# Kernel tuning notes

Hardware: AMD Instinct MI355X
Metric: run time of the kernel (lower is better)

The kernel has to match this reference:

```python
import jax, jax.numpy as jnp
import numpy as np

N_EVENTS = 16384
B = 4
H = W = 64
KH = KW = 3
P = KH * KW
D = 256  # input_size == hidden_size


def setup_inputs() -> dict:
    rng = np.random.default_rng(0)
    # events sorted by batch, time = arange (sorted within batch)
    batch_id = np.sort(rng.integers(0, B, N_EVENTS))
    hh = rng.integers(KH - 1, H - KH + 1, N_EVENTS)  # interior pixels -> exactly P patches each
    ww = rng.integers(KW - 1, W - KW + 1, N_EVENTS)
    time = np.arange(N_EVENTS)
    # scatter each event to its P=kh*kw overlapping patches (stride 1)
    Hp, Wp = H - KH + 1, W - KW + 1
    ki = np.arange(KH)[:, None]
    kj = np.arange(KW)[None, :]
    pos = (ki * KW + kj).reshape(1, P)                       # [1, P]
    pl = hh[:, None] - ki.reshape(1, -1).repeat(KW, 1).reshape(1, P) if False else None
    ki_f = np.repeat(np.arange(KH), KW)                       # [P]
    kj_f = np.tile(np.arange(KW), KH)                         # [P]
    patch_row = hh[:, None] - ki_f[None, :]                   # [N, P]
    patch_col = ww[:, None] - kj_f[None, :]
    patch_lin = (batch_id[:, None] * (Hp * Wp) + patch_row * Wp + patch_col).reshape(-1)
    pos_flat = np.broadcast_to((ki_f * KW + kj_f)[None, :], (N_EVENTS, P)).reshape(-1)
    orig_flat = np.repeat(np.arange(N_EVENTS), P)
    t_flat = np.repeat(time, P)
    order = np.lexsort((t_flat, patch_lin))                   # group by patch, time-ordered within
    patch_sorted = patch_lin[order]
    orig_event_idx = orig_flat[order].astype(np.int32)
    pos_id = pos_flat[order].astype(np.int32)
    seg_start = np.concatenate([[True], patch_sorted[1:] != patch_sorted[:-1]])

    key = jax.random.key(0)
    ks = jax.random.split(key, 8)
    std = np.sqrt(2.0 / (D + D)).astype(np.float32)
    lin = 1.0 / np.sqrt(D).astype(np.float32)
    return {
        "events": jax.random.normal(ks[0], (N_EVENTS, D), jnp.float32),
        "scatter_w": jax.random.normal(ks[1], (P, D, D), jnp.float32) * std,
        "gather_w": jax.random.normal(ks[2], (P, D, D), jnp.float32) * std,
        "q_w": jax.random.normal(ks[3], (D, D), jnp.float32) * lin,
        "v_w": jax.random.normal(ks[4], (D, D), jnp.float32) * lin,
        "g_w": jax.random.normal(ks[5], (D, D), jnp.float32) * lin,
        "o_w": jax.random.normal(ks[6], (D, D), jnp.float32) * lin,
        "ln_gamma": jnp.ones((D,), jnp.float32),
        "ln_beta": jnp.zeros((D,), jnp.float32),
        "orig_event_idx": jnp.asarray(orig_event_idx),
        "pos_id": jnp.asarray(pos_id),
        "seg_start": jnp.asarray(seg_start),
    }


def _pos_proj(x, weights, pos_id):
    # per-patch-position linear: out[n] = weights[pos_id[n]] @ x[n]
    # disjoint masks partition rows, so masked GEMMs sum exactly (mirrors torch loop)
    out = jnp.zeros((x.shape[0], weights.shape[1]), x.dtype)
    for i in range(weights.shape[0]):
        m = (pos_id == i)[:, None]
        out = out + jnp.where(m, x @ weights[i].T, 0.0)
    return out


def _gated_scan(g, v, seg_start):
    # h_t = g_t * h_{t-1} + (1 - g_t) * v_t, reset at segment starts
    a = jnp.where(seg_start[:, None], 0.0, g)
    b = (1.0 - g) * v
    def comb(c1, c2):
        a1, b1 = c1
        a2, b2 = c2
        return (a1 * a2, a2 * b1 + b2)
    _, h = jax.lax.associative_scan(comb, (a, b), axis=0)
    return h


def reference(events, scatter_w, gather_w, q_w, v_w, g_w, o_w, ln_gamma, ln_beta,
              orig_event_idx, pos_id, seg_start):
    x = events[orig_event_idx]                     # [M, D] scatter events -> patch copies
    y = _pos_proj(x, scatter_w, pos_id)            # indexed conv-like projection
    q = y @ q_w.T
    v = y @ v_w.T
    g = jax.nn.sigmoid(y @ g_w.T)
    h = _gated_scan(g, v, seg_start)               # ragged gated linear scan
    o = (q * h) @ o_w.T
    z = _pos_proj(o, gather_w, pos_id)             # indexed gather projection
    out = jnp.zeros_like(events).at[orig_event_idx].add(z)  # gather back (sum over P copies)
    out = out + events                             # residual (input_size == hidden_size)
    mu = jnp.mean(out, axis=-1, keepdims=True)
    var = jnp.mean(jnp.square(out - mu), axis=-1, keepdims=True)
    out = (out - mu) * jax.lax.rsqrt(var + 1e-5) * ln_gamma + ln_beta
    return out
```

## Files before the change

### kernel.cpp

```cpp
#include <hip/hip_runtime.h>

typedef __bf16 bf16x8 __attribute__((ext_vector_type(8)));
typedef float f32x4 __attribute__((ext_vector_type(4)));

#define NEV 16384
#define MTOT 147456
#define LDQ 2304
#define LDX 6912

__device__ __forceinline__ unsigned short f2bf(float f) {
  unsigned x = __float_as_uint(f);
  x += 0x7FFFu + ((x >> 16) & 1u);
  return (unsigned short)(x >> 16);
}
__device__ __forceinline__ float bf2f(unsigned short u) {
  return __uint_as_float(((unsigned)u) << 16);
}
__device__ __forceinline__ void load_lds16(const void* g, void* l) {
  __builtin_amdgcn_global_load_lds(
      (const __attribute__((address_space(1))) unsigned int*)g,
      (__attribute__((address_space(3))) unsigned int*)l, 16, 0, 0);
}

__global__ void k_cast4(const float* __restrict__ in, unsigned short* __restrict__ out, int n4) {
  int i = blockIdx.x * blockDim.x + threadIdx.x;
  if (i >= n4) return;
  float4 v = reinterpret_cast<const float4*>(in)[i];
  ushort4 o;
  o.x = f2bf(v.x); o.y = f2bf(v.y); o.z = f2bf(v.z); o.w = f2bf(v.w);
  reinterpret_cast<ushort4*>(out)[i] = o;
}

__global__ void k_cast3(const float* __restrict__ q, const float* __restrict__ v,
                        const float* __restrict__ g, unsigned short* __restrict__ out) {
  int which = blockIdx.y;
  const float* src = (which == 0) ? q : (which == 1) ? v : g;
  int i = blockIdx.x * blockDim.x + threadIdx.x;
  if (i >= 16384) return;
  float4 val = reinterpret_cast<const float4*>(src)[i];
  ushort4 o;
  o.x = f2bf(val.x); o.y = f2bf(val.y); o.z = f2bf(val.z); o.w = f2bf(val.w);
  reinterpret_cast<ushort4*>(out + (long)which * 65536)[i] = o;
}

__global__ void k_transpose(const float* __restrict__ in, unsigned short* __restrict__ out, int total) {
  int i = blockIdx.x * blockDim.x + threadIdx.x;
  if (i >= total) return;
  int b = i >> 16, r = (i >> 8) & 255, c = i & 255;
  out[i] = f2bf(in[((long)b << 16) + (c << 8) + r]);
}

__global__ void k_detect(const unsigned int* __restrict__ seg, int* mode) {
  __shared__ int fFloat, fGt1;
  if (threadIdx.x == 0) { fFloat = 0; fGt1 = 0; }
  __syncthreads();
  int lf = 0, lg = 0;
  for (int i = threadIdx.x; i < 1024; i += 256) {
    unsigned v = seg[i];
    if (v == 0x3F800000u) lf = 1;
    else if (v > 1u) lg = 1;
  }
  if (lf) atomicOr(&fFloat, 1);
  if (lg) atomicOr(&fGt1, 1);
  __syncthreads();
  if (threadIdx.x == 0) *mode = fFloat ? 2 : (fGt1 ? 1 : 0);
}

__device__ __forceinline__ bool is_start(const void* seg, int mode, int i) {
  if (mode == 1) return ((const unsigned char*)seg)[i] != 0;
  if (mode == 2) return ((const float*)seg)[i] != 0.0f;
  return ((const int*)seg)[i] != 0;
}

__global__ void k_compact(const void* __restrict__ seg, const int* __restrict__ mode,
                          int* counter, int* starts) {
  int i = blockIdx.x * blockDim.x + threadIdx.x;
  if (i >= MTOT) return;
  if (is_start(seg, *mode, i)) {
    int k = atomicAdd(counter, 1);
    starts[k] = i;
  }
}

template<bool F32OUT>
__device__ __forceinline__ void gemm_tile(
    const unsigned short* __restrict__ A, const unsigned short* __restrict__ B,
    void* __restrict__ Cv, const float* __restrict__ resid,
    int r0, int c0, int K, int lda, int ldb, int ldc,
    unsigned short* As, unsigned short* Bs) {
  const int tid = threadIdx.x, lane = tid & 63, wid = tid >> 6;
  const int wr = (wid >> 1) * 64, wc = (wid & 1) * 64;
  const int la = lane & 15, lb2 = lane >> 4;
  const int arow = tid >> 2;
  const int cs = ((tid & 3) ^ ((arow >> 1) & 3)) * 8;
  const int nk = K >> 5;
  f32x4 acc[4][4];
#pragma unroll
  for (int i = 0; i < 4; ++i)
#pragma unroll
    for (int j = 0; j < 4; ++j) acc[i][j] = (f32x4)0.0f;

  const unsigned short* ga0 = A + (long)(r0 + arow) * lda + cs;
  const unsigned short* gb0 = B + (long)(c0 + arow) * ldb + cs;

  load_lds16(ga0, &As[tid * 8]);
  load_lds16(ga0 + (long)64 * lda, &As[2048 + tid * 8]);
  load_lds16(gb0, &Bs[tid * 8]);
  load_lds16(gb0 + (long)64 * ldb, &Bs[2048 + tid * 8]);
  __syncthreads();

  for (int k = 0; k < nk; ++k) {
    if (k + 1 < nk) {
      const int nb = ((k + 1) & 1) * 4096;
      const unsigned short* ga = ga0 + (k + 1) * 32;
      const unsigned short* gb = gb0 + (k + 1) * 32;
      load_lds16(ga, &As[nb + tid * 8]);
      load_lds16(ga + (long)64 * lda, &As[nb + 2048 + tid * 8]);
      load_lds16(gb, &Bs[nb + tid * 8]);
      load_lds16(gb + (long)64 * ldb, &Bs[nb + 2048 + tid * 8]);
    }
    const int cb = (k & 1) * 4096;
    bf16x8 af[4], bv[4];
#pragma unroll
    for (int i = 0; i < 4; ++i) {
      const int ra = wr + i * 16 + la;
      const int rb = wc + i * 16 + la;
      af[i] = *reinterpret_cast<const bf16x8*>(&As[cb + ra * 32 + ((lb2 ^ ((ra >> 1) & 3)) * 8)]);
      bv[i] = *reinterpret_cast<const bf16x8*>(&Bs[cb + rb * 32 + ((lb2 ^ ((rb >> 1) & 3)) * 8)]);
    }
#pragma unroll
    for (int i = 0; i < 4; ++i)
#pragma unroll
      for (int j = 0; j < 4; ++j)
        acc[i][j] = __builtin_amdgcn_mfma_f32_16x16x32_bf16(af[i], bv[j], acc[i][j], 0, 0, 0);
    __syncthreads();
  }
#pragma unroll
  for (int i = 0; i < 4; ++i)
#pragma unroll
    for (int j = 0; j < 4; ++j)
#pragma unroll
      for (int r = 0; r < 4; ++r) {
        const int row = r0 + wr + i * 16 + lb2 * 4 + r;
        const int col = c0 + wc + j * 16 + la;
        if (F32OUT) {
          float v = acc[i][j][r];
          if (resid) v += resid[(long)row * ldc + col];
          ((float*)Cv)[(long)row * ldc + col] = v;
        } else {
          ((unsigned short*)Cv)[(long)row * ldc + col] = f2bf(acc[i][j][r]);
        }
      }
}

__global__ __launch_bounds__(256) void k_wgemm(
    const unsigned short* __restrict__ qvgw, const unsigned short* __restrict__ wt,
    const unsigned short* __restrict__ gaw, const unsigned short* __restrict__ owt,
    unsigned short* __restrict__ ABig, unsigned short* __restrict__ Bo2) {
  __shared__ __align__(16) unsigned short As[8192];
  __shared__ __align__(16) unsigned short Bs[8192];
  const int b = blockIdx.z;
  const unsigned short *A, *B;
  unsigned short* C;
  int ldc;
  if (b < 27) {
    A = qvgw + (long)(b / 9) * 65536;
    B = wt + (long)(b % 9) * 65536;
    C = ABig + (long)b * 65536; ldc = 256;
  } else {
    A = gaw + (long)(b - 27) * 65536;
    B = owt;
    C = Bo2 + (b - 27) * 256; ldc = LDQ;
  }
  gemm_tile<false>(A, B, C, nullptr, blockIdx.x * 128, blockIdx.y * 128, 256, 256, 256, ldc, As, Bs);
}

__global__ __launch_bounds__(256) void k_qvg3(
    const unsigned short* __restrict__ ev, const unsigned short* __restrict__ ABig,
    unsigned short* __restrict__ X) {
  __shared__ __align__(16) unsigned short As[4096];
  __shared__ __align__(16) unsigned short Bs[3][2048];
  const int p = blockIdx.z;
  const int r0 = blockIdx.x * 128, c0 = blockIdx.y * 64;
  const int tid = threadIdx.x, lane = tid & 63, wid = tid >> 6;
  const int wr2 = (wid >> 1) * 64, wc2 = (wid & 1) * 32;
  const int la = lane & 15, lb2 = lane >> 4;
  f32x4 acc[3][4][2];
#pragma unroll
  for (int w = 0; w < 3; ++w)
#pragma unroll
    for (int i = 0; i < 4; ++i)
#pragma unroll
      for (int j = 0; j < 2; ++j) acc[w][i][j] = (f32x4)0.0f;

  for (int k0 = 0; k0 < 256; k0 += 32) {
#pragma unroll
    for (int q = 0; q < 2; ++q) {
      const int g = q * 256 + tid;
      const int row = g >> 2, c = g & 3;
      load_lds16(ev + (long)(r0 + row) * 256 + k0 + ((c ^ ((row >> 1) & 3)) * 8), &As[g * 8]);
    }
#pragma unroll
    for (int w = 0; w < 3; ++w) {
      const unsigned short* Bw = ABig + (long)(w * 9 + p) * 65536;
      const int row = tid >> 2, c = tid & 3;
      load_lds16(Bw + (long)(c0 + row) * 256 + k0 + ((c ^ ((row >> 1) & 3)) * 8), &Bs[w][tid * 8]);
    }
    __syncthreads();
    bf16x8 af[4], bv[3][2];
#pragma unroll
    for (int i = 0; i < 4; ++i) {
      const int ra = wr2 + i * 16 + la;
      af[i] = *reinterpret_cast<const bf16x8*>(&As[ra * 32 + ((lb2 ^ ((ra >> 1) & 3)) * 8)]);
    }
#pragma unroll
    for (int w = 0; w < 3; ++w)
#pragma unroll
      for (int j = 0; j < 2; ++j) {
        const int rb = wc2 + j * 16 + la;
        bv[w][j] = *reinterpret_cast<const bf16x8*>(&Bs[w][rb * 32 + ((lb2 ^ ((rb >> 1) & 3)) * 8)]);
      }
#pragma unroll
    for (int w = 0; w < 3; ++w)
#pragma unroll
      for (int i = 0; i < 4; ++i)
#pragma unroll
        for (int j = 0; j < 2; ++j)
          acc[w][i][j] = __builtin_amdgcn_mfma_f32_16x16x32_bf16(af[i], bv[w][j], acc[w][i][j], 0, 0, 0);
    __syncthreads();
  }
#pragma unroll
  for (int w = 0; w < 3; ++w) {
    unsigned short* Xw = X + p * 768 + w * 256;
#pragma unroll
    for (int i = 0; i < 4; ++i)
#pragma unroll
      for (int j = 0; j < 2; ++j)
#pragma unroll
        for (int r = 0; r < 4; ++r) {
          const int row = r0 + wr2 + i * 16 + lb2 * 4 + r;
          const int col = c0 + wc2 + j * 16 + la;
          Xw[(long)row * LDX + col] = f2bf(acc[w][i][j][r]);
        }
  }
}

__global__ __launch_bounds__(256) void k_scan(
    unsigned short* __restrict__ X,
    const int* __restrict__ starts, const int* __restrict__ cntp, const int* __restrict__ modep,
    const void* __restrict__ seg, const int* __restrict__ pos_id, const int* __restrict__ oidx) {
  const int lane = threadIdx.x & 63;
  const int w = blockIdx.x * 4 + (threadIdx.x >> 6);
  const int nW = gridDim.x * 4;
  const int nseg = *cntp;
  const int md = *modep;
  for (int s = w; s < nseg; s += nW) {
    int t = starts[s];
    int p = pos_id[t], e = oidx[t];
    long base = (long)e * LDX + p * 768 + lane * 4;
    ushort4 ql = *(const ushort4*)(X + base);
    ushort4 vl = *(const ushort4*)(X + base + 256);
    ushort4 gl = *(const ushort4*)(X + base + 512);
    bool cont = (t + 1 < MTOT) && !is_start(seg, md, t + 1);
    float h0 = 0.f, h1 = 0.f, h2 = 0.f, h3 = 0.f;
    for (;;) {
      ushort4 qn, vn, gn;
      long nbase = 0;
      bool cont2 = false;
      if (cont) {
        int pn = pos_id[t + 1], en = oidx[t + 1];
        nbase = (long)en * LDX + pn * 768 + lane * 4;
        qn = *(const ushort4*)(X + nbase);
        vn = *(const ushort4*)(X + nbase + 256);
        gn = *(const ushort4*)(X + nbase + 512);
        cont2 = (t + 2 < MTOT) && !is_start(seg, md, t + 2);
      }
      float g0 = 1.f / (1.f + __expf(-bf2f(gl.x)));
      float g1 = 1.f / (1.f + __expf(-bf2f(gl.y)));
      float g2 = 1.f / (1.f + __expf(-bf2f(gl.z)));
      float g3 = 1.f / (1.f + __expf(-bf2f(gl.w)));
      h0 = g0 * h0 + (1.f - g0) * bf2f(vl.x);
      h1 = g1 * h1 + (1.f - g1) * bf2f(vl.y);
      h2 = g2 * h2 + (1.f - g2) * bf2f(vl.z);
      h3 = g3 * h3 + (1.f - g3) * bf2f(vl.w);
      ushort4 o;
      o.x = f2bf(bf2f(ql.x) * h0);
      o.y = f2bf(bf2f(ql.y) * h1);
      o.z = f2bf(bf2f(ql.z) * h2);
      o.w = f2bf(bf2f(ql.w) * h3);
      *(ushort4*)(X + base + 256) = o;
      if (!cont) break;
      ++t;
      base = nbase; ql = qn; vl = vn; gl = gn; cont = cont2;
    }
  }
}

__global__ __launch_bounds__(256) void k_p5(
    const unsigned short* __restrict__ X, const unsigned short* __restrict__ Bo2,
    const float* __restrict__ ev, float* __restrict__ S) {
  __shared__ __align__(16) unsigned short As[4096];
  __shared__ __align__(16) unsigned short Bs[4096];
  const int r0 = blockIdx.x * 128, c0 = blockIdx.y * 128;
  const int tid = threadIdx.x, lane = tid & 63, wid = tid >> 6;
  const int wr = (wid >> 1) * 64, wc = (wid & 1) * 64;
  const int la = lane & 15, lb2 = lane >> 4;
  const int arow = tid >> 2;
  const int cs = ((tid & 3) ^ ((arow >> 1) & 3)) * 8;
  f32x4 acc[4][4];
#pragma unroll
  for (int i = 0; i < 4; ++i)
#pragma unroll
    for (int j = 0; j < 4; ++j) acc[i][j] = (f32x4)0.0f;

  for (int kc = 0; kc < 72; ++kc) {
    const int p = kc >> 3, nn = (kc & 7) * 32;
    const unsigned short* ga = X + (long)(r0 + arow) * LDX + p * 768 + 256 + nn + cs;
    const unsigned short* gb = Bo2 + (long)(c0 + arow) * LDQ + p * 256 + nn + cs;
    load_lds16(ga, &As[tid * 8]);
    load_lds16(ga + (long)64 * LDX, &As[2048 + tid * 8]);
    load_lds16(gb, &Bs[tid * 8]);
    load_lds16(gb + (long)64 * LDQ, &Bs[2048 + tid * 8]);
    __syncthreads();
    bf16x8 af[4], bv[4];
#pragma unroll
    for (int i = 0; i < 4; ++i) {
      const int ra = wr + i * 16 + la;
      const int rb = wc + i * 16 + la;
      af[i] = *reinterpret_cast<const bf16x8*>(&As[ra * 32 + ((lb2 ^ ((ra >> 1) & 3)) * 8)]);
      bv[i] = *reinterpret_cast<const bf16x8*>(&Bs[rb * 32 + ((lb2 ^ ((rb >> 1) & 3)) * 8)]);
    }
#pragma unroll
    for (int i = 0; i < 4; ++i)
#pragma unroll
      for (int j = 0; j < 4; ++j)
        acc[i][j] = __builtin_amdgcn_mfma_f32_16x16x32_bf16(af[i], bv[j], acc[i][j], 0, 0, 0);
    __syncthreads();
  }
#pragma unroll
  for (int i = 0; i < 4; ++i)
#pragma unroll
    for (int j = 0; j < 4; ++j)
#pragma unroll
      for (int r = 0; r < 4; ++r) {
        const int row = r0 + wr + i * 16 + lb2 * 4 + r;
        const int col = c0 + wc + j * 16 + la;
        S[(long)row * 256 + col] = acc[i][j][r] + ev[(long)row * 256 + col];
      }
}

__global__ __launch_bounds__(256) void k_ln(float* __restrict__ S,
                                            const float* __restrict__ gamma, const float* __restrict__ beta) {
  int row = blockIdx.x * 4 + (threadIdx.x >> 6);
  int lane = threadIdx.x & 63;
  long base = (long)row * 256 + lane * 4;
  float4 s4 = *reinterpret_cast<const float4*>(S + base);
  float v0 = s4.x, v1 = s4.y, v2 = s4.z, v3 = s4.w;
  float s = v0 + v1 + v2 + v3;
  float ss = v0 * v0 + v1 * v1 + v2 * v2 + v3 * v3;
  for (int o = 32; o; o >>= 1) { s += __shfl_xor(s, o, 64); ss += __shfl_xor(ss, o, 64); }
  float mu = s * (1.0f / 256.0f);
  float var = ss * (1.0f / 256.0f) - mu * mu;
  float rs = rsqrtf(fmaxf(var, 0.0f) + 1e-5f);
  float4 g4 = *reinterpret_cast<const float4*>(gamma + lane * 4);
  float4 b4 = *reinterpret_cast<const float4*>(beta + lane * 4);
  float4 o4;
  o4.x = (v0 - mu) * rs * g4.x + b4.x;
  o4.y = (v1 - mu) * rs * g4.y + b4.y;
  o4.z = (v2 - mu) * rs * g4.z + b4.z;
  o4.w = (v3 - mu) * rs * g4.w + b4.w;
  *reinterpret_cast<float4*>(S + base) = o4;
}

extern "C" void kernel_launch(void* const* d_in, const int* in_sizes, int n_in,
                              void* d_out, int out_size, void* d_ws, size_t ws_size,
                              hipStream_t stream) {
  const float* events    = (const float*)d_in[0];
  const float* scatter_w = (const float*)d_in[1];
  const float* gather_w  = (const float*)d_in[2];
  const float* q_w       = (const float*)d_in[3];
  const float* v_w       = (const float*)d_in[4];
  const float* g_w       = (const float*)d_in[5];
  const float* o_w       = (const float*)d_in[6];
  const float* ln_gamma  = (const float*)d_in[7];
  const float* ln_beta   = (const float*)d_in[8];
  const int*   oidx      = (const int*)d_in[9];
  const int*   pos_id    = (const int*)d_in[10];
  const void*  seg       = d_in[11];
  float* out = (float*)d_out;

  char* base = (char*)d_ws;
  int* counter = (int*)base;
  int* mode    = (int*)(base + 4);
  int* starts  = (int*)(base + 256);
  unsigned short* ev_bf  = (unsigned short*)(base + 590080);
  unsigned short* wt     = (unsigned short*)(base + 8978688);
  unsigned short* qvgw   = (unsigned short*)(base + 10158336);
  unsigned short* owt    = (unsigned short*)(base + 10551552);
  unsigned short* gaw_bf = (unsigned short*)(base + 10682624);
  unsigned short* ABig   = (unsigned short*)(base + 11862272);
  unsigned short* Bo2    = (unsigned short*)(base + 15401216);
  unsigned short* X      = (unsigned short*)(base + 16580864);

  hipMemsetAsync(counter, 0, 8, stream);
  k_detect<<<1, 256, 0, stream>>>((const unsigned int*)seg, mode);

  k_cast4<<<4096, 256, 0, stream>>>(events, ev_bf, 1048576);
  k_cast3<<<dim3(64, 3), 256, 0, stream>>>(q_w, v_w, g_w, qvgw);
  k_cast4<<<576, 256, 0, stream>>>(gather_w, gaw_bf, 147456);
  k_transpose<<<2304, 256, 0, stream>>>(scatter_w, wt, 589824);
  k_transpose<<<256, 256, 0, stream>>>(o_w, owt, 65536);

  k_wgemm<<<dim3(2, 2, 36), 256, 0, stream>>>(qvgw, wt, gaw_bf, owt, ABig, Bo2);

  k_qvg3<<<dim3(128, 4, 9), 256, 0, stream>>>(ev_bf, ABig, X);

  k_compact<<<576, 256, 0, stream>>>(seg, mode, counter, starts);
  k_scan<<<2048, 256, 0, stream>>>(X, starts, counter, mode, seg, pos_id, oidx);

  k_p5<<<dim3(128, 2), 256, 0, stream>>>(X, Bo2, events, out);
  k_ln<<<4096, 256, 0, stream>>>(out, ln_gamma, ln_beta);
}
```

Before: 271.3 us.

## Tile weight transposes, make segment compaction ordered, and widen qvg3 K-step

Replaces the naive strided weight transpose with a 32x32 LDS-tiled transpose so both reads and writes are coalesced. Replaces the atomic segment-start compaction with a two-pass ballot/popcount count-and-emit that writes starts in sorted order and drops the memset. Doubles the k_qvg3 K tile to 64 with a new XOR swizzle, halving barriers per tile at the cost of twice the LDS. Ordered starts may also improve locality in the scan kernel.

```diff
diff --git a/kernel.cpp b/kernel.cpp
--- a/kernel.cpp
+++ b/kernel.cpp
@@ -43,11 +43,21 @@
   reinterpret_cast<ushort4*>(out + (long)which * 65536)[i] = o;
 }
 
-__global__ void k_transpose(const float* __restrict__ in, unsigned short* __restrict__ out, int total) {
-  int i = blockIdx.x * blockDim.x + threadIdx.x;
-  if (i >= total) return;
-  int b = i >> 16, r = (i >> 8) & 255, c = i & 255;
-  out[i] = f2bf(in[((long)b << 16) + (c << 8) + r]);
+__global__ __launch_bounds__(256) void k_transpose_t(const float* __restrict__ in,
+                                                     unsigned short* __restrict__ out) {
+  __shared__ float s[32][33];
+  const int b = blockIdx.z;
+  const int r0 = blockIdx.x * 32, c0 = blockIdx.y * 32;
+  const int tx = threadIdx.x & 31, ty = threadIdx.x >> 5;
+  const float* src = in + (long)b * 65536;
+  unsigned short* dst = out + (long)b * 65536;
+#pragma unroll
+  for (int cc = 0; cc < 4; ++cc)
+    s[ty + cc * 8][tx] = src[(c0 + ty + cc * 8) * 256 + r0 + tx];
+  __syncthreads();
+#pragma unroll
+  for (int cc = 0; cc < 4; ++cc)
+    dst[(long)(r0 + ty + cc * 8) * 256 + c0 + tx] = f2bf(s[tx][ty + cc * 8]);
 }
 
 __global__ void k_detect(const unsigned int* __restrict__ seg, int* mode) {
@@ -72,21 +82,58 @@
   return ((const int*)seg)[i] != 0;
 }
 
-__global__ void k_compact(const void* __restrict__ seg, const int* __restrict__ mode,
-                          int* counter, int* starts) {
-  int i = blockIdx.x * blockDim.x + threadIdx.x;
-  if (i >= MTOT) return;
-  if (is_start(seg, *mode, i)) {
-    int k = atomicAdd(counter, 1);
-    starts[k] = i;
+__global__ __launch_bounds__(256) void k_count(const void* __restrict__ seg,
+                                               const int* __restrict__ modep,
+                                               int* __restrict__ blockCounts) {
+  __shared__ int wc[4];
+  const int md = *modep;
+  const int i = blockIdx.x * 256 + threadIdx.x;
+  const bool f = is_start(seg, md, i);
+  unsigned long long m = __ballot(f);
+  const int lane = threadIdx.x & 63, wid = threadIdx.x >> 6;
+  if (lane == 0) wc[wid] = __popcll(m);
+  __syncthreads();
+  if (threadIdx.x == 0) blockCounts[blockIdx.x] = wc[0] + wc[1] + wc[2] + wc[3];
+}
+
+__global__ __launch_bounds__(256) void k_emit(const void* __restrict__ seg,
+                                              const int* __restrict__ modep,
+                                              const int* __restrict__ blockCounts,
+                                              int* __restrict__ starts, int* __restrict__ nsegp) {
+  __shared__ int sh[12];
+  const int md = *modep;
+  const int bid = blockIdx.x, tid = threadIdx.x;
+  const int lane = tid & 63, wid = tid >> 6;
+  int part = 0;
+  for (int j = tid; j < bid; j += 256) part += blockCounts[j];
+  for (int o = 32; o; o >>= 1) part += __shfl_xor(part, o, 64);
+  if (lane == 0) sh[wid] = part;
+  if (bid == 0) {
+    int tot = 0;
+    for (int j = tid; j < 576; j += 256) tot += blockCounts[j];
+    for (int o = 32; o; o >>= 1) tot += __shfl_xor(tot, o, 64);
+    if (lane == 0) sh[8 + wid] = tot;
+  }
+  const int i = bid * 256 + tid;
+  const bool f = is_start(seg, md, i);
+  unsigned long long m = __ballot(f);
+  if (lane == 0) sh[4 + wid] = __popcll(m);
+  __syncthreads();
+  const int base = sh[0] + sh[1] + sh[2] + sh[3];
+  int wpre = 0;
+#pragma unroll
+  for (int w2 = 0; w2 < 4; ++w2) if (w2 < wid) wpre += sh[4 + w2];
+  if (bid == 0 && tid == 0) *nsegp = sh[8] + sh[9] + sh[10] + sh[11];
+  if (f) {
+    const int lanePre = __popcll(m & ((1ull << lane) - 1));
+    starts[base + wpre + lanePre] = i;
   }
 }
 
 template<bool F32OUT>
 __device__ __forceinline__ void gemm_tile(
     const unsigned short* __restrict__ A, const unsigned short* __restrict__ B,
-    void* __restrict__ Cv, const float* __restrict__ resid,
-    int r0, int c0, int K, int lda, int ldb, int ldc,
+    void* __restrict__ Cv, int r0, int c0, int K, int lda, int ldb, int ldc,
     unsigned short* As, unsigned short* Bs) {
   const int tid = threadIdx.x, lane = tid & 63, wid = tid >> 6;
   const int wr = (wid >> 1) * 64, wc = (wid & 1) * 64;
@@ -143,13 +190,8 @@
       for (int r = 0; r < 4; ++r) {
         const int row = r0 + wr + i * 16 + lb2 * 4 + r;
         const int col = c0 + wc + j * 16 + la;
-        if (F32OUT) {
-          float v = acc[i][j][r];
-          if (resid) v += resid[(long)row * ldc + col];
-          ((float*)Cv)[(long)row * ldc + col] = v;
-        } else {
-          ((unsigned short*)Cv)[(long)row * ldc + col] = f2bf(acc[i][j][r]);
-        }
+        if (F32OUT) ((float*)Cv)[(long)row * ldc + col] = acc[i][j][r];
+        else ((unsigned short*)Cv)[(long)row * ldc + col] = f2bf(acc[i][j][r]);
       }
 }
 
@@ -172,14 +214,14 @@
     B = owt;
     C = Bo2 + (b - 27) * 256; ldc = LDQ;
   }
-  gemm_tile<false>(A, B, C, nullptr, blockIdx.x * 128, blockIdx.y * 128, 256, 256, 256, ldc, As, Bs);
+  gemm_tile<false>(A, B, C, blockIdx.x * 128, blockIdx.y * 128, 256, 256, 256, ldc, As, Bs);
 }
 
 __global__ __launch_bounds__(256) void k_qvg3(
     const unsigned short* __restrict__ ev, const unsigned short* __restrict__ ABig,
     unsigned short* __restrict__ X) {
-  __shared__ __align__(16) unsigned short As[4096];
-  __shared__ __align__(16) unsigned short Bs[3][2048];
+  __shared__ __align__(16) unsigned short As[8192];
+  __shared__ __align__(16) unsigned short Bs[3][4096];
   const int p = blockIdx.z;
   const int r0 = blockIdx.x * 128, c0 = blockIdx.y * 64;
   const int tid = threadIdx.x, lane = tid & 63, wid = tid >> 6;
@@ -193,40 +235,49 @@
 #pragma unroll
       for (int j = 0; j < 2; ++j) acc[w][i][j] = (f32x4)0.0f;
 
-  for (int k0 = 0; k0 < 256; k0 += 32) {
-#pragma unroll
-    for (int q = 0; q < 2; ++q) {
+  for (int k0 = 0; k0 < 256; k0 += 64) {
+#pragma unroll
+    for (int q = 0; q < 4; ++q) {
       const int g = q * 256 + tid;
-      const int row = g >> 2, c = g & 3;
-      load_lds16(ev + (long)(r0 + row) * 256 + k0 + ((c ^ ((row >> 1) & 3)) * 8), &As[g * 8]);
+      const int row = g >> 3, c = g & 7;
+      load_lds16(ev + (long)(r0 + row) * 256 + k0 + ((c ^ (row & 7)) * 8), &As[g * 8]);
     }
 #pragma unroll
     for (int w = 0; w < 3; ++w) {
       const unsigned short* Bw = ABig + (long)(w * 9 + p) * 65536;
-      const int row = tid >> 2, c = tid & 3;
-      load_lds16(Bw + (long)(c0 + row) * 256 + k0 + ((c ^ ((row >> 1) & 3)) * 8), &Bs[w][tid * 8]);
+#pragma unroll
+      for (int q = 0; q < 2; ++q) {
+        const int g = q * 256 + tid;
+        const int row = g >> 3, c = g & 7;
+        load_lds16(Bw + (long)(c0 + row) * 256 + k0 + ((c ^ (row & 7)) * 8), &Bs[w][g * 8]);
+      }
     }
     __syncthreads();
-    bf16x8 af[4], bv[3][2];
-#pragma unroll
-    for (int i = 0; i < 4; ++i) {
-      const int ra = wr2 + i * 16 + la;
-      af[i] = *reinterpret_cast<const bf16x8*>(&As[ra * 32 + ((lb2 ^ ((ra >> 1) & 3)) * 8)]);
-    }
-#pragma unroll
-    for (int w = 0; w < 3; ++w)
-#pragma unroll
-      for (int j = 0; j < 2; ++j) {
-        const int rb = wc2 + j * 16 + la;
-        bv[w][j] = *reinterpret_cast<const bf16x8*>(&Bs[w][rb * 32 + ((lb2 ^ ((rb >> 1) & 3)) * 8)]);
+#pragma unroll
+    for (int kk = 0; kk < 2; ++kk) {
+      bf16x8 af[4], bv[3][2];
+#pragma unroll
+      for (int i = 0; i < 4; ++i) {
+        const int ra = wr2 + i * 16 + la;
+        const int slot = (kk * 4 + lb2) ^ (ra & 7);
+        af[i] = *reinterpret_cast<const bf16x8*>(&As[ra * 64 + slot * 8]);
       }
 #pragma unroll
-    for (int w = 0; w < 3; ++w)
-#pragma unroll
-      for (int i = 0; i < 4; ++i)
-#pragma unroll
-        for (int j = 0; j < 2; ++j)
-          acc[w][i][j] = __builtin_amdgcn_mfma_f32_16x16x32_bf16(af[i], bv[w][j], acc[w][i][j], 0, 0, 0);
+      for (int w = 0; w < 3; ++w)
+#pragma unroll
+        for (int j = 0; j < 2; ++j) {
+          const int rb = wc2 + j * 16 + la;
+          const int slot = (kk * 4 + lb2) ^ (rb & 7);
+          bv[w][j] = *reinterpret_cast<const bf16x8*>(&Bs[w][rb * 64 + slot * 8]);
+        }
+#pragma unroll
+      for (int w = 0; w < 3; ++w)
+#pragma unroll
+        for (int i = 0; i < 4; ++i)
+#pragma unroll
+          for (int j = 0; j < 2; ++j)
+            acc[w][i][j] = __builtin_amdgcn_mfma_f32_16x16x32_bf16(af[i], bv[w][j], acc[w][i][j], 0, 0, 0);
+    }
     __syncthreads();
   }
 #pragma unroll
@@ -392,30 +443,31 @@
   char* base = (char*)d_ws;
   int* counter = (int*)base;
   int* mode    = (int*)(base + 4);
-  int* starts  = (int*)(base + 256);
-  unsigned short* ev_bf  = (unsigned short*)(base + 590080);
-  unsigned short* wt     = (unsigned short*)(base + 8978688);
-  unsigned short* qvgw   = (unsigned short*)(base + 10158336);
-  unsigned short* owt    = (unsigned short*)(base + 10551552);
-  unsigned short* gaw_bf = (unsigned short*)(base + 10682624);
-  unsigned short* ABig   = (unsigned short*)(base + 11862272);
-  unsigned short* Bo2    = (unsigned short*)(base + 15401216);
-  unsigned short* X      = (unsigned short*)(base + 16580864);
-
-  hipMemsetAsync(counter, 0, 8, stream);
+  int* blockCounts = (int*)(base + 64);
+  int* starts  = (int*)(base + 4096);
+  unsigned short* ev_bf  = (unsigned short*)(base + 598016);
+  unsigned short* wt     = (unsigned short*)(base + 8986624);
+  unsigned short* qvgw   = (unsigned short*)(base + 10166272);
+  unsigned short* owt    = (unsigned short*)(base + 10559488);
+  unsigned short* gaw_bf = (unsigned short*)(base + 10690560);
+  unsigned short* ABig   = (unsigned short*)(base + 11870208);
+  unsigned short* Bo2    = (unsigned short*)(base + 15409152);
+  unsigned short* X      = (unsigned short*)(base + 16588800);
+
   k_detect<<<1, 256, 0, stream>>>((const unsigned int*)seg, mode);
 
   k_cast4<<<4096, 256, 0, stream>>>(events, ev_bf, 1048576);
   k_cast3<<<dim3(64, 3), 256, 0, stream>>>(q_w, v_w, g_w, qvgw);
   k_cast4<<<576, 256, 0, stream>>>(gather_w, gaw_bf, 147456);
-  k_transpose<<<2304, 256, 0, stream>>>(scatter_w, wt, 589824);
-  k_transpose<<<256, 256, 0, stream>>>(o_w, owt, 65536);
+  k_transpose_t<<<dim3(8, 8, 9), 256, 0, stream>>>(scatter_w, wt);
+  k_transpose_t<<<dim3(8, 8, 1), 256, 0, stream>>>(o_w, owt);
 
   k_wgemm<<<dim3(2, 2, 36), 256, 0, stream>>>(qvgw, wt, gaw_bf, owt, ABig, Bo2);
 
   k_qvg3<<<dim3(128, 4, 9), 256, 0, stream>>>(ev_bf, ABig, X);
 
-  k_compact<<<576, 256, 0, stream>>>(seg, mode, counter, starts);
+  k_count<<<576, 256, 0, stream>>>(seg, mode, blockCounts);
+  k_emit<<<576, 256, 0, stream>>>(seg, mode, blockCounts, starts, counter);
   k_scan<<<2048, 256, 0, stream>>>(X, starts, counter, mode, seg, pos_id, oidx);
 
   k_p5<<<dim3(128, 2), 256, 0, stream>>>(X, Bo2, events, out);
```

Measured after the change: 228.3 us. 15.8% less time.
